# Kernel optimization log

Hardware: AMD Instinct MI355X
Metric: run time of the kernel (lower is better)

## Reference

```python
import jax, jax.numpy as jnp
import numpy as np

EPS = 1e-12

def setup_inputs() -> dict:
    key = jax.random.key(0)
    k1, k2, k3, k4, k5, k6 = jax.random.split(key, 6)
    B, DIM, T = 16, 256, 2048
    K, D = 1024, 64  # num_embeddings, embedding_dim
    N = B * T
    input_data = jax.random.normal(k1, (B, DIM, T), dtype=jnp.float32)
    codebooks = jax.random.normal(k2, (K, D), dtype=jnp.float32)
    W_in = jax.random.normal(k3, (DIM, D), dtype=jnp.float32) / np.sqrt(DIM)
    b_in = jnp.zeros((D,), dtype=jnp.float32)
    W_out = jax.random.normal(k4, (D, DIM), dtype=jnp.float32) / np.sqrt(D)
    b_out = jnp.zeros((DIM,), dtype=jnp.float32)
    random_vector = jax.random.normal(k5, (N, D), dtype=jnp.float32)
    return {"input_data": input_data, "codebooks": codebooks,
            "W_in": W_in, "b_in": b_in, "W_out": W_out, "b_out": b_out,
            "random_vector": random_vector}

def reference(input_data, codebooks, W_in, b_in, W_out, b_out, random_vector):
    B, DIM, T = input_data.shape
    D = codebooks.shape[1]
    # encode: [B, DIM, T] -> [B, T, DIM] -> project -> [B*T, D]
    x = jnp.einsum('bct,cd->btd', input_data, W_in) + b_in
    x = x.reshape(-1, D)  # [N, D]
    distances = (jnp.sum(x * x, axis=1, keepdims=True)
                 - 2.0 * (x @ codebooks.T)
                 + jnp.sum(codebooks * codebooks, axis=1)[None, :])  # [N, K]
    min_indices = jnp.argmin(distances, axis=1)  # [N]
    hard = codebooks[min_indices]  # [N, D]
    # noise substitution
    norm_resid = jnp.sqrt(jnp.sum((x - hard) ** 2, axis=1, keepdims=True))
    norm_rand = jnp.sqrt(jnp.sum(random_vector ** 2, axis=1, keepdims=True))
    vq_error = (norm_resid / (norm_rand + EPS)) * random_vector
    q = x + vq_error  # [N, D]
    # decode: [N, D] -> [B, T, D] -> project_out -> [B, DIM, T]
    q = q.reshape(B, T, D)
    out = jnp.einsum('btd,dc->bct', q, W_out) + b_out[None, :, None]
    return out
```

## Files before the change

### kernel.cpp

```cpp
#include <hip/hip_runtime.h>
#include <hip/hip_bf16.h>

typedef __bf16 bf16x8 __attribute__((ext_vector_type(8)));
typedef unsigned short u16x8 __attribute__((ext_vector_type(8)));
typedef unsigned int u32x2 __attribute__((ext_vector_type(2)));
typedef unsigned int u32x4 __attribute__((ext_vector_type(4)));
typedef float f32x4 __attribute__((ext_vector_type(4)));
typedef unsigned short u16;

constexpr int DIMc = 256, Tt = 2048, Dd = 64;

__device__ __forceinline__ u16 f2b(float f) {
  unsigned u = __float_as_uint(f);
  return (u16)((u + 0x7FFFu + ((u >> 16) & 1u)) >> 16);
}
__device__ __forceinline__ float b2f(u16 v) {
  return __uint_as_float(((unsigned)v) << 16);
}
__device__ __forceinline__ unsigned f2b2(float a, float b) {
  return (unsigned)f2b(a) | ((unsigned)f2b(b) << 16);
}
__device__ __forceinline__ f32x4 mfma16(u16x8 a, u16x8 b, f32x4 c) {
  return __builtin_amdgcn_mfma_f32_16x16x32_bf16(
      __builtin_bit_cast(bf16x8, a), __builtin_bit_cast(bf16x8, b), c, 0, 0, 0);
}

__global__ __launch_bounds__(256, 2) void nsvq_fused(
    const float* __restrict__ in, const float* __restrict__ rnd,
    const float* __restrict__ cb, const float* __restrict__ Win,
    const float* __restrict__ bin, const float* __restrict__ Wout,
    const float* __restrict__ bout, float* __restrict__ out) {
  __shared__ u16 sm[39424];
  u16* const WinT = sm;
  u16* const WoX  = sm;
  u16* const InT  = sm + 18432;
  u16* const Xt   = sm + 34816;
  float* const mnp = (float*)(sm + 38912);

  const int tid  = threadIdx.x;
  const int lane = tid & 63;
  const int w    = tid >> 6;
  const int quad = lane >> 4, col = lane & 15;
  const int b    = blockIdx.x >> 5;
  const int t0   = (blockIdx.x & 31) << 6;
  const int myt  = w * 16 + col;

  {
    const int c = tid;
    #pragma unroll
    for (int k = 0; k < 8; ++k) {
      const int d0 = k * 8;
      const float4* wr = (const float4*)(Win + c * 64 + d0);
      float4 v0 = wr[0], v1 = wr[1];
      u16* dst = WinT + c;
      dst[(d0 + 0) * 288] = f2b(v0.x); dst[(d0 + 1) * 288] = f2b(v0.y);
      dst[(d0 + 2) * 288] = f2b(v0.z); dst[(d0 + 3) * 288] = f2b(v0.w);
      dst[(d0 + 4) * 288] = f2b(v1.x); dst[(d0 + 5) * 288] = f2b(v1.y);
      dst[(d0 + 6) * 288] = f2b(v1.z); dst[(d0 + 7) * 288] = f2b(v1.w);
    }
  }
  {
    const int t = tid & 63, cg = tid >> 6;
    const float* ib = in + (size_t)b * DIMc * Tt + t0 + t;
    #pragma unroll
    for (int it = 0; it < 8; ++it) {
      const int c0 = cg * 8 + it * 32;
      u32x4 pk;
      #pragma unroll
      for (int jj = 0; jj < 4; ++jj)
        pk[jj] = f2b2(ib[(size_t)(c0 + 2 * jj) * Tt], ib[(size_t)(c0 + 2 * jj + 1) * Tt]);
      *(u32x4*)(InT + t * 256 + (((c0 >> 3) ^ (t & 7)) << 3)) = pk;
    }
  }
  float rr2v = 0.f, rv[16];
  const float* rb = rnd + ((size_t)b * Tt + t0) * Dd;
  #pragma unroll
  for (int tt = 0; tt < 16; ++tt) {
    rv[tt] = rb[(size_t)(w * 16 + tt) * Dd + lane];
    float s = rv[tt] * rv[tt];
    s += __shfl_xor(s, 1);  s += __shfl_xor(s, 2);  s += __shfl_xor(s, 4);
    s += __shfl_xor(s, 8);  s += __shfl_xor(s, 16); s += __shfl_xor(s, 32);
    if (col == tt) rr2v = s;
  }
  __syncthreads();

  f32x4 acc[4];
  {
    u16x8 Bf[8];
    #pragma unroll
    for (int kt = 0; kt < 8; ++kt)
      Bf[kt] = *(const u16x8*)(InT + myt * 256 + (((kt * 4 + quad) ^ (myt & 7)) << 3));
    #pragma unroll
    for (int mt = 0; mt < 4; ++mt) {
      float4 bi = *(const float4*)(bin + mt * 16 + quad * 4);
      f32x4 a = {bi.x, bi.y, bi.z, bi.w};
      #pragma unroll
      for (int kt = 0; kt < 8; ++kt) {
        u16x8 A = *(const u16x8*)(WinT + (mt * 16 + col) * 288 + kt * 32 + quad * 8);
        a = mfma16(A, Bf[kt], a);
      }
      acc[mt] = a;
    }
  }
  float x2v = 0.f;
  #pragma unroll
  for (int mt = 0; mt < 4; ++mt) {
    #pragma unroll
    for (int r = 0; r < 4; ++r) x2v = fmaf(acc[mt][r], acc[mt][r], x2v);
    u32x2 px = { f2b2(acc[mt][0], acc[mt][1]), f2b2(acc[mt][2], acc[mt][3]) };
    const int bk  = mt * 2 + (quad >> 1);
    const int off = myt * 64 + ((bk ^ (myt & 7)) << 3) + (quad & 1) * 4;
    *(u32x2*)(Xt + off) = px;
  }
  x2v += __shfl_xor(x2v, 16);
  x2v += __shfl_xor(x2v, 32);
  __syncthreads();

  {
    const int c = tid;
    #pragma unroll
    for (int k = 0; k < 8; ++k) {
      const int d0 = k * 8;
      u32x4 pk;
      #pragma unroll
      for (int jj = 0; jj < 4; ++jj)
        pk[jj] = f2b2(Wout[(size_t)(d0 + 2 * jj) * 256 + c],
                      Wout[(size_t)(d0 + 2 * jj + 1) * 256 + c]);
      *(u32x4*)(WoX + c * 72 + d0) = pk;
    }
  }
  u16x8 Xa[4], Xb[4];
  #pragma unroll
  for (int nt = 0; nt < 4; ++nt) {
    const int tr = nt * 16 + col;
    Xa[nt] = *(const u16x8*)(Xt + tr * 64 + ((quad ^ (tr & 7)) << 3));
    Xb[nt] = *(const u16x8*)(Xt + tr * 64 + (((4 + quad) ^ (tr & 7)) << 3));
  }
  float minv[4];
  #pragma unroll
  for (int i = 0; i < 4; ++i) minv[i] = 3.4e38f;
  const float* cw = cb + (size_t)(w * 256) * Dd;
  for (int mi = 0; mi < 16; ++mi) {
    const float* cr = cw + (size_t)(mi * 16 + col) * Dd + quad * 8;
    float4 c0 = ((const float4*)cr)[0],        c1 = ((const float4*)cr)[1];
    float4 c2 = ((const float4*)(cr + 32))[0], c3 = ((const float4*)(cr + 32))[1];
    float cnA = fmaf(c0.w, c0.w, fmaf(c0.z, c0.z, fmaf(c0.y, c0.y, c0.x * c0.x)));
    float cnB = fmaf(c1.w, c1.w, fmaf(c1.z, c1.z, fmaf(c1.y, c1.y, c1.x * c1.x)));
    float cnC = fmaf(c2.w, c2.w, fmaf(c2.z, c2.z, fmaf(c2.y, c2.y, c2.x * c2.x)));
    float cnD = fmaf(c3.w, c3.w, fmaf(c3.z, c3.z, fmaf(c3.y, c3.y, c3.x * c3.x)));
    float cn = (cnA + cnB) + (cnC + cnD);
    cn += __shfl_xor(cn, 16); cn += __shfl_xor(cn, 32);
    f32x4 cn4;
    #pragma unroll
    for (int r = 0; r < 4; ++r) cn4[r] = __shfl(cn, quad * 4 + r);
    u32x4 a0 = { f2b2(-2.f * c0.x, -2.f * c0.y), f2b2(-2.f * c0.z, -2.f * c0.w),
                 f2b2(-2.f * c1.x, -2.f * c1.y), f2b2(-2.f * c1.z, -2.f * c1.w) };
    u32x4 a1 = { f2b2(-2.f * c2.x, -2.f * c2.y), f2b2(-2.f * c2.z, -2.f * c2.w),
                 f2b2(-2.f * c3.x, -2.f * c3.y), f2b2(-2.f * c3.z, -2.f * c3.w) };
    u16x8 A0 = __builtin_bit_cast(u16x8, a0);
    u16x8 A1 = __builtin_bit_cast(u16x8, a1);
    #pragma unroll
    for (int nt = 0; nt < 4; ++nt) {
      f32x4 a = mfma16(A0, Xa[nt], cn4);
      a = mfma16(A1, Xb[nt], a);
      #pragma unroll
      for (int r = 0; r < 4; ++r) minv[nt] = fminf(minv[nt], a[r]);
    }
  }
  #pragma unroll
  for (int nt = 0; nt < 4; ++nt) {
    float m = minv[nt];
    m = fminf(m, __shfl_xor(m, 16));
    m = fminf(m, __shfl_xor(m, 32));
    mnp[w * 64 + nt * 16 + col] = m;
  }
  __syncthreads();

  float mv = 3.4e38f;
  #pragma unroll
  for (int j = 0; j < 4; ++j) mv = fminf(mv, mnp[j * 64 + myt]);
  float r2  = fmaxf(x2v + mv, 0.f);
  float scv = sqrtf(r2) / (sqrtf(rr2v) + 1e-12f);
  #pragma unroll
  for (int tt = 0; tt < 16; ++tt) {
    float s  = __shfl(scv, tt);
    const int tr  = w * 16 + tt;
    const int idx = tr * 64 + (((lane >> 3) ^ (tr & 7)) << 3) + (lane & 7);
    Xt[idx] = f2b(fmaf(s, rv[tt], b2f(Xt[idx])));
  }

  u16x8 Q0 = *(const u16x8*)(Xt + myt * 64 + ((quad ^ (myt & 7)) << 3));
  u16x8 Q1 = *(const u16x8*)(Xt + myt * 64 + (((4 + quad) ^ (myt & 7)) << 3));
  float* ob0 = out + (size_t)b * DIMc * Tt + t0 + myt;
  #pragma unroll
  for (int mt = 0; mt < 16; ++mt) {
    const u16* ar = WoX + (mt * 16 + col) * 72;
    u16x8 A0 = *(const u16x8*)(ar + quad * 8);
    u16x8 A1 = *(const u16x8*)(ar + 32 + quad * 8);
    float4 bo = *(const float4*)(bout + mt * 16 + quad * 4);
    f32x4 a = {bo.x, bo.y, bo.z, bo.w};
    a = mfma16(A0, Q0, a);
    a = mfma16(A1, Q1, a);
    float* ob = ob0 + (size_t)(mt * 16 + quad * 4) * Tt;
    #pragma unroll
    for (int r = 0; r < 4; ++r) ob[(size_t)r * Tt] = a[r];
  }
}

extern "C" void kernel_launch(void* const* d_in, const int* in_sizes, int n_in,
                              void* d_out, int out_size, void* d_ws, size_t ws_size,
                              hipStream_t stream) {
  const float *in = nullptr, *cbp = nullptr, *rnd = nullptr, *bin = nullptr, *bout = nullptr;
  const float* w16[2] = {nullptr, nullptr}; int nw = 0;
  for (int i = 0; i < n_in; ++i) {
    switch (in_sizes[i]) {
      case 8388608: in  = (const float*)d_in[i]; break;
      case 65536:   cbp = (const float*)d_in[i]; break;
      case 2097152: rnd = (const float*)d_in[i]; break;
      case 64:      bin = (const float*)d_in[i]; break;
      case 256:     bout= (const float*)d_in[i]; break;
      case 16384:   if (nw < 2) w16[nw++] = (const float*)d_in[i]; break;
      default: break;
    }
  }
  if (!in)   in  = (const float*)d_in[0];
  if (!cbp)  cbp = (const float*)d_in[1];
  if (nw < 2) { w16[0] = (const float*)d_in[2]; w16[1] = (const float*)d_in[4]; }
  if (!bin)  bin = (const float*)d_in[3];
  if (!bout) bout = (const float*)d_in[5];
  if (!rnd)  rnd = (const float*)d_in[6];

  nsvq_fused<<<512, 256, 0, stream>>>(in, rnd, cbp, w16[0], bin, w16[1], bout, (float*)d_out);
}
```

Before: 121.6 us.

## Precompute bf16 weights and codebook norms in prep kernel, DMA into LDS

Adds a small prep kernel that converts the codebook (pre-scaled by -2), its squared norms, and swizzled transposed W_in/W_out to bf16 in the workspace. The main kernel then loads these with direct global-to-LDS DMA instead of converting per block, and loads input straight into registers rather than staging it through LDS. This cuts LDS usage enough to allow 3 blocks per CU. The aim is to remove redundant per-block conversion and norm work and to raise occupancy, at the cost of an extra kernel launch and a workspace dependency between the two kernels.

After: 115.8 us. -4.8%, faster.

```diff
diff --git a/kernel.cpp b/kernel.cpp
--- a/kernel.cpp
+++ b/kernel.cpp
@@ -4,11 +4,15 @@
 typedef __bf16 bf16x8 __attribute__((ext_vector_type(8)));
 typedef unsigned short u16x8 __attribute__((ext_vector_type(8)));
 typedef unsigned int u32x2 __attribute__((ext_vector_type(2)));
-typedef unsigned int u32x4 __attribute__((ext_vector_type(4)));
 typedef float f32x4 __attribute__((ext_vector_type(4)));
 typedef unsigned short u16;
 
 constexpr int DIMc = 256, Tt = 2048, Dd = 64;
+
+#define CBF_U  0
+#define CN_U   65536
+#define WINT_U 67584
+#define WOX_U  83968
 
 __device__ __forceinline__ u16 f2b(float f) {
   unsigned u = __float_as_uint(f);
@@ -24,18 +28,56 @@
   return __builtin_amdgcn_mfma_f32_16x16x32_bf16(
       __builtin_bit_cast(bf16x8, a), __builtin_bit_cast(bf16x8, b), c, 0, 0, 0);
 }
-
-__global__ __launch_bounds__(256, 2) void nsvq_fused(
+__device__ __forceinline__ void dma16(const u16* g, u16* l) {
+  __builtin_amdgcn_global_load_lds(
+      (const __attribute__((address_space(1))) unsigned int*)g,
+      (__attribute__((address_space(3))) unsigned int*)l, 16, 0, 0);
+}
+
+__global__ void nsvq_prep(const float* __restrict__ cb, const float* __restrict__ Win,
+                          const float* __restrict__ Wout, u16* __restrict__ wsu) {
+  const int g = blockIdx.x * 256 + threadIdx.x;
+  {
+    const int k = g >> 4, j = (g & 15) << 2;
+    float4 v = *(const float4*)(cb + k * 64 + j);
+    u16* row = wsu + CBF_U + k * 64 + j;
+    row[0] = f2b(-2.f * v.x); row[1] = f2b(-2.f * v.y);
+    row[2] = f2b(-2.f * v.z); row[3] = f2b(-2.f * v.w);
+  }
+  if (g < 1024) {
+    const float* cr = cb + g * 64;
+    float p[4];
+    #pragma unroll
+    for (int q = 0; q < 4; ++q) {
+      float4 a0 = ((const float4*)(cr + q * 8))[0],      a1 = ((const float4*)(cr + q * 8))[1];
+      float4 a2 = ((const float4*)(cr + 32 + q * 8))[0], a3 = ((const float4*)(cr + 32 + q * 8))[1];
+      float pA = fmaf(a0.w, a0.w, fmaf(a0.z, a0.z, fmaf(a0.y, a0.y, a0.x * a0.x)));
+      float pB = fmaf(a1.w, a1.w, fmaf(a1.z, a1.z, fmaf(a1.y, a1.y, a1.x * a1.x)));
+      float pC = fmaf(a2.w, a2.w, fmaf(a2.z, a2.z, fmaf(a2.y, a2.y, a2.x * a2.x)));
+      float pD = fmaf(a3.w, a3.w, fmaf(a3.z, a3.z, fmaf(a3.y, a3.y, a3.x * a3.x)));
+      p[q] = (pA + pB) + (pC + pD);
+    }
+    ((float*)(wsu + CN_U))[g] = (p[0] + p[1]) + (p[2] + p[3]);
+  }
+  {
+    const int d = g >> 8, c = g & 255;
+    wsu[WINT_U + d * 256 + (((c >> 3) ^ (d & 7)) << 3) + (c & 7)] = f2b(Win[c * 64 + d]);
+  }
+  {
+    const int c = g >> 6, d = g & 63;
+    wsu[WOX_U + c * 64 + (((d >> 3) ^ (c & 7)) << 3) + (d & 7)] = f2b(Wout[d * 256 + c]);
+  }
+}
+
+__global__ __launch_bounds__(256, 3) void nsvq_main(
     const float* __restrict__ in, const float* __restrict__ rnd,
-    const float* __restrict__ cb, const float* __restrict__ Win,
-    const float* __restrict__ bin, const float* __restrict__ Wout,
-    const float* __restrict__ bout, float* __restrict__ out) {
-  __shared__ u16 sm[39424];
+    const float* __restrict__ bin, const float* __restrict__ bout,
+    const u16* __restrict__ wsu, float* __restrict__ out) {
+  __shared__ u16 sm[20992];
   u16* const WinT = sm;
   u16* const WoX  = sm;
-  u16* const InT  = sm + 18432;
-  u16* const Xt   = sm + 34816;
-  float* const mnp = (float*)(sm + 38912);
+  u16* const Xt   = sm + 16384;
+  float* const mnp = (float*)(sm + 20480);
 
   const int tid  = threadIdx.x;
   const int lane = tid & 63;
@@ -45,32 +87,22 @@
   const int t0   = (blockIdx.x & 31) << 6;
   const int myt  = w * 16 + col;
 
-  {
-    const int c = tid;
-    #pragma unroll
-    for (int k = 0; k < 8; ++k) {
-      const int d0 = k * 8;
-      const float4* wr = (const float4*)(Win + c * 64 + d0);
-      float4 v0 = wr[0], v1 = wr[1];
-      u16* dst = WinT + c;
-      dst[(d0 + 0) * 288] = f2b(v0.x); dst[(d0 + 1) * 288] = f2b(v0.y);
-      dst[(d0 + 2) * 288] = f2b(v0.z); dst[(d0 + 3) * 288] = f2b(v0.w);
-      dst[(d0 + 4) * 288] = f2b(v1.x); dst[(d0 + 5) * 288] = f2b(v1.y);
-      dst[(d0 + 6) * 288] = f2b(v1.z); dst[(d0 + 7) * 288] = f2b(v1.w);
-    }
-  }
-  {
-    const int t = tid & 63, cg = tid >> 6;
-    const float* ib = in + (size_t)b * DIMc * Tt + t0 + t;
-    #pragma unroll
-    for (int it = 0; it < 8; ++it) {
-      const int c0 = cg * 8 + it * 32;
-      u32x4 pk;
-      #pragma unroll
-      for (int jj = 0; jj < 4; ++jj)
-        pk[jj] = f2b2(ib[(size_t)(c0 + 2 * jj) * Tt], ib[(size_t)(c0 + 2 * jj + 1) * Tt]);
-      *(u32x4*)(InT + t * 256 + (((c0 >> 3) ^ (t & 7)) << 3)) = pk;
-    }
+  #pragma unroll
+  for (int ii = 0; ii < 8; ++ii) {
+    const int i = w + 4 * ii;
+    dma16(wsu + WINT_U + i * 512 + lane * 8, WinT + i * 512);
+  }
+  u16x8 Bf[8];
+  const float* ibase = in + (size_t)b * DIMc * Tt + t0 + myt;
+  #pragma unroll
+  for (int kt = 0; kt < 8; ++kt) {
+    float v[8];
+    #pragma unroll
+    for (int j = 0; j < 8; ++j) v[j] = ibase[(size_t)(kt * 32 + quad * 8 + j) * Tt];
+    u16x8 pk;
+    #pragma unroll
+    for (int j = 0; j < 8; ++j) pk[j] = f2b(v[j]);
+    Bf[kt] = pk;
   }
   float rr2v = 0.f, rv[16];
   const float* rb = rnd + ((size_t)b * Tt + t0) * Dd;
@@ -85,22 +117,17 @@
   __syncthreads();
 
   f32x4 acc[4];
-  {
-    u16x8 Bf[8];
-    #pragma unroll
-    for (int kt = 0; kt < 8; ++kt)
-      Bf[kt] = *(const u16x8*)(InT + myt * 256 + (((kt * 4 + quad) ^ (myt & 7)) << 3));
-    #pragma unroll
-    for (int mt = 0; mt < 4; ++mt) {
-      float4 bi = *(const float4*)(bin + mt * 16 + quad * 4);
-      f32x4 a = {bi.x, bi.y, bi.z, bi.w};
-      #pragma unroll
-      for (int kt = 0; kt < 8; ++kt) {
-        u16x8 A = *(const u16x8*)(WinT + (mt * 16 + col) * 288 + kt * 32 + quad * 8);
-        a = mfma16(A, Bf[kt], a);
-      }
-      acc[mt] = a;
-    }
+  #pragma unroll
+  for (int mt = 0; mt < 4; ++mt) {
+    float4 bi = *(const float4*)(bin + mt * 16 + quad * 4);
+    f32x4 a = {bi.x, bi.y, bi.z, bi.w};
+    const int d = mt * 16 + col;
+    #pragma unroll
+    for (int kt = 0; kt < 8; ++kt) {
+      u16x8 A = *(const u16x8*)(WinT + d * 256 + (((kt * 4 + quad) ^ (d & 7)) << 3));
+      a = mfma16(A, Bf[kt], a);
+    }
+    acc[mt] = a;
   }
   float x2v = 0.f;
   #pragma unroll
@@ -116,18 +143,10 @@
   x2v += __shfl_xor(x2v, 32);
   __syncthreads();
 
-  {
-    const int c = tid;
-    #pragma unroll
-    for (int k = 0; k < 8; ++k) {
-      const int d0 = k * 8;
-      u32x4 pk;
-      #pragma unroll
-      for (int jj = 0; jj < 4; ++jj)
-        pk[jj] = f2b2(Wout[(size_t)(d0 + 2 * jj) * 256 + c],
-                      Wout[(size_t)(d0 + 2 * jj + 1) * 256 + c]);
-      *(u32x4*)(WoX + c * 72 + d0) = pk;
-    }
+  #pragma unroll
+  for (int ii = 0; ii < 8; ++ii) {
+    const int i = w + 4 * ii;
+    dma16(wsu + WOX_U + i * 512 + lane * 8, WoX + i * 512);
   }
   u16x8 Xa[4], Xb[4];
   #pragma unroll
@@ -139,26 +158,13 @@
   float minv[4];
   #pragma unroll
   for (int i = 0; i < 4; ++i) minv[i] = 3.4e38f;
-  const float* cw = cb + (size_t)(w * 256) * Dd;
+  const u16* cwf   = wsu + CBF_U + (size_t)(w * 256) * 64;
+  const float* cnp = (const float*)(wsu + CN_U) + w * 256;
+  #pragma unroll 4
   for (int mi = 0; mi < 16; ++mi) {
-    const float* cr = cw + (size_t)(mi * 16 + col) * Dd + quad * 8;
-    float4 c0 = ((const float4*)cr)[0],        c1 = ((const float4*)cr)[1];
-    float4 c2 = ((const float4*)(cr + 32))[0], c3 = ((const float4*)(cr + 32))[1];
-    float cnA = fmaf(c0.w, c0.w, fmaf(c0.z, c0.z, fmaf(c0.y, c0.y, c0.x * c0.x)));
-    float cnB = fmaf(c1.w, c1.w, fmaf(c1.z, c1.z, fmaf(c1.y, c1.y, c1.x * c1.x)));
-    float cnC = fmaf(c2.w, c2.w, fmaf(c2.z, c2.z, fmaf(c2.y, c2.y, c2.x * c2.x)));
-    float cnD = fmaf(c3.w, c3.w, fmaf(c3.z, c3.z, fmaf(c3.y, c3.y, c3.x * c3.x)));
-    float cn = (cnA + cnB) + (cnC + cnD);
-    cn += __shfl_xor(cn, 16); cn += __shfl_xor(cn, 32);
-    f32x4 cn4;
-    #pragma unroll
-    for (int r = 0; r < 4; ++r) cn4[r] = __shfl(cn, quad * 4 + r);
-    u32x4 a0 = { f2b2(-2.f * c0.x, -2.f * c0.y), f2b2(-2.f * c0.z, -2.f * c0.w),
-                 f2b2(-2.f * c1.x, -2.f * c1.y), f2b2(-2.f * c1.z, -2.f * c1.w) };
-    u32x4 a1 = { f2b2(-2.f * c2.x, -2.f * c2.y), f2b2(-2.f * c2.z, -2.f * c2.w),
-                 f2b2(-2.f * c3.x, -2.f * c3.y), f2b2(-2.f * c3.z, -2.f * c3.w) };
-    u16x8 A0 = __builtin_bit_cast(u16x8, a0);
-    u16x8 A1 = __builtin_bit_cast(u16x8, a1);
+    u16x8 A0 = *(const u16x8*)(cwf + (mi * 16 + col) * 64 + quad * 8);
+    u16x8 A1 = *(const u16x8*)(cwf + (mi * 16 + col) * 64 + 32 + quad * 8);
+    f32x4 cn4 = *(const f32x4*)(cnp + mi * 16 + quad * 4);
     #pragma unroll
     for (int nt = 0; nt < 4; ++nt) {
       f32x4 a = mfma16(A0, Xa[nt], cn4);
@@ -194,9 +200,10 @@
   float* ob0 = out + (size_t)b * DIMc * Tt + t0 + myt;
   #pragma unroll
   for (int mt = 0; mt < 16; ++mt) {
-    const u16* ar = WoX + (mt * 16 + col) * 72;
-    u16x8 A0 = *(const u16x8*)(ar + quad * 8);
-    u16x8 A1 = *(const u16x8*)(ar + 32 + quad * 8);
+    const int c = mt * 16 + col;
+    const u16* ar = WoX + c * 64;
+    u16x8 A0 = *(const u16x8*)(ar + ((quad ^ (c & 7)) << 3));
+    u16x8 A1 = *(const u16x8*)(ar + (((4 + quad) ^ (c & 7)) << 3));
     float4 bo = *(const float4*)(bout + mt * 16 + quad * 4);
     f32x4 a = {bo.x, bo.y, bo.z, bo.w};
     a = mfma16(A0, Q0, a);
@@ -230,5 +237,7 @@
   if (!bout) bout = (const float*)d_in[5];
   if (!rnd)  rnd = (const float*)d_in[6];
 
-  nsvq_fused<<<512, 256, 0, stream>>>(in, rnd, cbp, w16[0], bin, w16[1], bout, (float*)d_out);
-}
+  u16* wsu = (u16*)d_ws;
+  nsvq_prep<<<64, 256, 0, stream>>>(cbp, w16[0], w16[1], wsu);
+  nsvq_main<<<512, 256, 0, stream>>>(in, rnd, bin, bout, wsu, (float*)d_out);
+}
```
